# Kernel tuning notes

Measured on AMD Instinct MI355X. Metric: run time of the kernel, lower is better.

## Reference

```python
import jax, jax.numpy as jnp
import numpy as np

B, N, K = 8, 4096, 16
N_STEPS = 4
DT = 0.05
EPS = 1e-8


def symmetrize(M):
    return 0.5 * (M + jnp.swapaxes(M, -1, -2))


def ensure_spd(S, eps):
    # Project to SPD cone via eigenvalue clipping: V max(L, eps) V^T
    Kd = S.shape[-1]
    S = symmetrize(S + eps * jnp.eye(Kd, dtype=S.dtype))
    w, U = jnp.linalg.eigh(S)
    w = jnp.clip(w, eps, None)
    return symmetrize((U * w[..., None, :]) @ jnp.swapaxes(U, -1, -2))


def spd_exponential_map(Sigma, V, eps=EPS):
    # exp_Sigma(V) = S^{1/2} exp(S^{-1/2} V S^{-1/2}) S^{1/2}
    Kd = Sigma.shape[-1]
    Sigma = symmetrize(Sigma) + eps * jnp.eye(Kd, dtype=Sigma.dtype)
    w, U = jnp.linalg.eigh(Sigma)
    w = jnp.clip(w, eps, None)
    sq = jnp.sqrt(w)
    Ut = jnp.swapaxes(U, -1, -2)
    S_sqrt = (U * sq[..., None, :]) @ Ut
    S_isqrt = (U * (1.0 / sq)[..., None, :]) @ Ut
    W = symmetrize(S_isqrt @ V @ S_isqrt)
    ww, Uw = jnp.linalg.eigh(W)
    ww = jnp.clip(ww, -20.0, 20.0)
    expW = (Uw * jnp.exp(ww)[..., None, :]) @ jnp.swapaxes(Uw, -1, -2)
    return ensure_spd(S_sqrt @ expW @ S_sqrt, eps)


def spd_kinetic_gradient(Sigma, pi_Sigma):
    # dT/dSigma = 2 pi Sigma pi, symmetrized
    return symmetrize(2.0 * (pi_Sigma @ Sigma) @ pi_Sigma)


def retract_to_principal_ball(phi, margin=0.01):
    eps = 1e-12
    r_max = jnp.pi - margin
    theta = jnp.linalg.norm(phi, axis=-1, keepdims=True)
    theta_safe = jnp.maximum(theta, eps)
    axis = phi / theta_safe
    two_pi = 2.0 * jnp.pi
    tw = jnp.remainder(theta, two_pi)
    flip = tw > jnp.pi
    tf = jnp.where(flip, two_pi - tw, tw)
    af = jnp.where(flip, -axis, axis)
    tf = jnp.minimum(tf, r_max)
    return af * tf


def setup_inputs() -> dict:
    key = jax.random.key(0)
    ks = jax.random.split(key, 7)
    mu = jax.random.normal(ks[0], (B, N, K), dtype=jnp.float32)
    A = 0.3 * jax.random.normal(ks[1], (B, N, K, K), dtype=jnp.float32)
    Sigma = A @ jnp.swapaxes(A, -1, -2) + jnp.eye(K, dtype=jnp.float32)
    phi = 0.5 * jax.random.normal(ks[2], (B, N, 3), dtype=jnp.float32)
    pi_mu = 0.1 * jax.random.normal(ks[3], (B, N, K), dtype=jnp.float32)
    pi_Sigma = symmetrize(0.05 * jax.random.normal(ks[4], (B, N, K, K), dtype=jnp.float32))
    pi_phi = 0.1 * jax.random.normal(ks[5], (B, N, 3), dtype=jnp.float32)
    Bm = 0.3 * jax.random.normal(ks[6], (B, N, K, K), dtype=jnp.float32)
    M_inv = Bm @ jnp.swapaxes(Bm, -1, -2) + jnp.eye(K, dtype=jnp.float32)
    return {"mu": mu, "Sigma": Sigma, "phi": phi,
            "pi_mu": pi_mu, "pi_Sigma": pi_Sigma, "pi_phi": pi_phi,
            "M_inv": M_inv}


def reference(mu, Sigma, phi, pi_mu, pi_Sigma, pi_phi, M_inv):
    dt = DT
    for _ in range(N_STEPS):  # fixed small leapfrog step count
        # half-step momentum kick from curved-geometry kinetic force
        pi_Sigma = symmetrize(pi_Sigma - 0.5 * dt * spd_kinetic_gradient(Sigma, pi_Sigma))
        # full-step position drift
        mu = mu + dt * jnp.einsum('bnij,bnj->bni', M_inv, pi_mu)
        Sigma_dot = 2.0 * Sigma @ pi_Sigma @ Sigma  # dSigma/dt from Legendre transform
        Sigma = spd_exponential_map(Sigma, dt * Sigma_dot, EPS)
        phi = retract_to_principal_ball(phi + dt * pi_phi)
        # second half-step momentum kick
        pi_Sigma = symmetrize(pi_Sigma - 0.5 * dt * spd_kinetic_gradient(Sigma, pi_Sigma))
    return (mu, Sigma, phi)
```

## Files before the change

### kernel.cpp

```cpp
#include <hip/hip_runtime.h>
#include <math.h>

typedef float f32x4 __attribute__((ext_vector_type(4)));
typedef _Float16 f16x4 __attribute__((ext_vector_type(4)));
typedef __fp16 fp16x2 __attribute__((ext_vector_type(2)));
typedef __fp16 fp16x4 __attribute__((ext_vector_type(4)));

#define MFMA_F16 __builtin_amdgcn_mfma_f32_16x16x16f16

namespace {
constexpr float DT = 0.05f;
constexpr int NSTEPS = 4;

struct Split { f16x4 h; f16x4 l; };

__device__ __forceinline__ f16x4 pk4(f32x4 v) {
  fp16x2 a = __builtin_amdgcn_cvt_pkrtz(v[0], v[1]);
  fp16x2 b = __builtin_amdgcn_cvt_pkrtz(v[2], v[3]);
  fp16x4 r = __builtin_shufflevector(a, b, 0, 1, 2, 3);
  return __builtin_bit_cast(f16x4, r);
}

__device__ __forceinline__ Split mksplit(f32x4 v) {
  Split s;
  s.h = pk4(v);
  f32x4 hf;
#pragma unroll
  for (int i = 0; i < 4; ++i) hf[i] = (float)s.h[i];
  s.l = pk4(v - hf);
  return s;
}

__device__ __forceinline__ f32x4 mm3(Split a, Split b) {
  f32x4 acc = {0.f, 0.f, 0.f, 0.f};
  acc = MFMA_F16(a.h, b.h, acc, 0, 0, 0);
  acc = MFMA_F16(a.h, b.l, acc, 0, 0, 0);
  acc = MFMA_F16(a.l, b.h, acc, 0, 0, 0);
  return acc;
}
__device__ __forceinline__ f32x4 mm2_acc(Split a, f16x4 bh, f32x4 acc0) {
  f32x4 acc = acc0;
  acc = MFMA_F16(a.h, bh, acc, 0, 0, 0);
  acc = MFMA_F16(a.l, bh, acc, 0, 0, 0);
  return acc;
}
__device__ __forceinline__ f32x4 mm1(f16x4 ah, f16x4 bh) {
  f32x4 acc = {0.f, 0.f, 0.f, 0.f};
  acc = MFMA_F16(ah, bh, acc, 0, 0, 0);
  return acc;
}
}

__global__ __launch_bounds__(256, 4) void ham_leapfrog(
    const float* __restrict__ mu, const float* __restrict__ Sigma,
    const float* __restrict__ phi, const float* __restrict__ pi_mu,
    const float* __restrict__ pi_Sigma, const float* __restrict__ pi_phi,
    const float* __restrict__ M_inv, float* __restrict__ out, int n_elem) {
  const int wave = threadIdx.x >> 6;
  const int lane = threadIdx.x & 63;
  const int e = blockIdx.x * (blockDim.x >> 6) + wave;
  if (e >= n_elem) return;

  const int c = lane & 15;
  const int r0 = (lane >> 4) * 4;
  const int eb = e * 256;
  const int ev = e * 16;

  f32x4 Sg, Dv, Mi;
#pragma unroll
  for (int j = 0; j < 4; ++j) {
    const int off = eb + (r0 + j) * 16 + c;
    Sg[j] = Sigma[off];
    Dv[j] = pi_Sigma[off];
    Mi[j] = M_inv[off];
  }
  Dv = (2.0f * DT) * Dv;

  f32x4 pm4 = *(const f32x4*)(pi_mu + ev + r0);
  f16x4 Ph = pk4(pm4);
  if (c != 0) Ph = (f16x4)(_Float16)0;
  f32x4 am = mm1(pk4(Mi), Ph);

  float p0 = phi[e * 3 + 0];
  float p1 = phi[e * 3 + 1];
  float p2 = phi[e * 3 + 2];
  const float q0 = DT * pi_phi[e * 3 + 0];
  const float q1 = DT * pi_phi[e * 3 + 1];
  const float q2 = DT * pi_phi[e * 3 + 2];
  const float TWO_PI = 6.28318530717958647692f;
  const float INV_2PI = 0.15915494309189533577f;
  const float PI_F = 3.14159265358979323846f;
  const float R_MAX = 3.13159265358979323846f;
#pragma unroll
  for (int s = 0; s < NSTEPS; ++s) {
    p0 += q0; p1 += q1; p2 += q2;
    float th = sqrtf(p0 * p0 + p1 * p1 + p2 * p2);
    float inv = __builtin_amdgcn_rcpf(fmaxf(th, 1e-12f));
    float tw = th - TWO_PI * floorf(th * INV_2PI);
    bool flip = tw > PI_F;
    float tf = flip ? (TWO_PI - tw) : tw;
    float sgn = flip ? -1.f : 1.f;
    tf = fminf(tf, R_MAX);
    float f = sgn * inv * tf;
    p0 *= f; p1 *= f; p2 *= f;
  }

  Split sS = mksplit(Sg);
  Split sD = mksplit(Dv);

#pragma unroll
  for (int step = 0; step < NSTEPS; ++step) {
    {
      f32x4 T = mm3(sS, sD);
      f16x4 Th = pk4(-0.5f * T);
      Dv = mm2_acc(sD, Th, Dv);
      sD = mksplit(Dv);
    }
    {
      f32x4 X = mm3(sD, sS);
      Split sX = mksplit(X);
      f32x4 Z = mm3(sS, sX);
      f32x4 ACC = Sg + Z;
      f16x4 zh = pk4(Z);
      Z = mm1(zh, sX.h); ACC += (1.0f / 2.0f) * Z; zh = pk4(Z);
      Z = mm1(zh, sX.h); ACC += (1.0f / 6.0f) * Z; zh = pk4(Z);
      Z = mm1(zh, sX.h); ACC += (1.0f / 24.0f) * Z;
      Sg = ACC;
      sS = mksplit(Sg);
    }
    {
      f32x4 T = mm3(sS, sD);
      f16x4 Th = pk4(-0.5f * T);
      Dv = mm2_acc(sD, Th, Dv);
      sD = mksplit(Dv);
    }
  }

  float* out_mu = out;
  float* out_Sg = out + (size_t)n_elem * 16;
  float* out_ph = out + (size_t)n_elem * (16 + 256);

#pragma unroll
  for (int j = 0; j < 4; ++j)
    out_Sg[eb + (r0 + j) * 16 + c] = Sg[j];

  if (c == 0) {
    f32x4 mu4 = *(const f32x4*)(mu + ev + r0);
    *(f32x4*)(out_mu + ev + r0) = mu4 + ((float)NSTEPS * DT) * am;
  }
  if (lane == 0) {
    out_ph[e * 3 + 0] = p0;
    out_ph[e * 3 + 1] = p1;
    out_ph[e * 3 + 2] = p2;
  }
}

extern "C" void kernel_launch(void* const* d_in, const int* in_sizes, int n_in,
                              void* d_out, int out_size, void* d_ws, size_t ws_size,
                              hipStream_t stream) {
  const float* mu       = (const float*)d_in[0];
  const float* Sigma    = (const float*)d_in[1];
  const float* phi      = (const float*)d_in[2];
  const float* pi_mu    = (const float*)d_in[3];
  const float* pi_Sigma = (const float*)d_in[4];
  const float* pi_phi   = (const float*)d_in[5];
  const float* M_inv    = (const float*)d_in[6];
  float* o = (float*)d_out;

  const int n_elem = in_sizes[0] / 16;
  const int waves_per_block = 4;
  const int blocks = (n_elem + waves_per_block - 1) / waves_per_block;
  hipLaunchKernelGGL(ham_leapfrog, dim3(blocks), dim3(256), 0, stream,
                     mu, Sigma, phi, pi_mu, pi_Sigma, pi_phi, M_inv, o, n_elem);
}
```

Measured before the change: 153.1 us.

## Process two matrices per wave and interleave their MFMA chains, trimming kick precision

Each wave now handles two independent 16x16 elements and alternates their kick and drift steps, so the two dependent MFMA chains can overlap and hide MFMA latency. The kick's first product drops the low-by-high correction term (3 MFMAs down to 2), slightly lowering precision. The mu update and phi retraction are moved and the phi work is split across two lanes. Register pressure roughly doubles, which may lower occupancy under the 256x4 launch bounds.

```diff
diff --git a/kernel.cpp b/kernel.cpp
--- a/kernel.cpp
+++ b/kernel.cpp
@@ -31,23 +31,44 @@
   return s;
 }
 
-__device__ __forceinline__ f32x4 mm3(Split a, Split b) {
-  f32x4 acc = {0.f, 0.f, 0.f, 0.f};
-  acc = MFMA_F16(a.h, b.h, acc, 0, 0, 0);
-  acc = MFMA_F16(a.h, b.l, acc, 0, 0, 0);
-  acc = MFMA_F16(a.l, b.h, acc, 0, 0, 0);
-  return acc;
-}
-__device__ __forceinline__ f32x4 mm2_acc(Split a, f16x4 bh, f32x4 acc0) {
-  f32x4 acc = acc0;
-  acc = MFMA_F16(a.h, bh, acc, 0, 0, 0);
-  acc = MFMA_F16(a.l, bh, acc, 0, 0, 0);
-  return acc;
-}
 __device__ __forceinline__ f32x4 mm1(f16x4 ah, f16x4 bh) {
   f32x4 acc = {0.f, 0.f, 0.f, 0.f};
   acc = MFMA_F16(ah, bh, acc, 0, 0, 0);
   return acc;
+}
+
+struct El {
+  f32x4 Sg, Dv;
+  Split sS, sD;
+};
+
+__device__ __forceinline__ void kick(El& E) {
+  f32x4 T = {0.f, 0.f, 0.f, 0.f};
+  T = MFMA_F16(E.sS.h, E.sD.h, T, 0, 0, 0);
+  T = MFMA_F16(E.sS.h, E.sD.l, T, 0, 0, 0);
+  f16x4 Th = pk4(-0.5f * T);
+  E.Dv = MFMA_F16(E.sD.h, Th, E.Dv, 0, 0, 0);
+  E.Dv = MFMA_F16(E.sD.l, Th, E.Dv, 0, 0, 0);
+  E.sD = mksplit(E.Dv);
+}
+
+__device__ __forceinline__ void drift(El& E) {
+  f32x4 X = {0.f, 0.f, 0.f, 0.f};
+  X = MFMA_F16(E.sD.h, E.sS.h, X, 0, 0, 0);
+  X = MFMA_F16(E.sD.l, E.sS.h, X, 0, 0, 0);
+  X = MFMA_F16(E.sD.h, E.sS.l, X, 0, 0, 0);
+  Split sX = mksplit(X);
+  f32x4 Z = {0.f, 0.f, 0.f, 0.f};
+  Z = MFMA_F16(E.sS.h, sX.h, Z, 0, 0, 0);
+  Z = MFMA_F16(E.sS.l, sX.h, Z, 0, 0, 0);
+  Z = MFMA_F16(E.sS.h, sX.l, Z, 0, 0, 0);
+  f32x4 ACC = E.Sg + Z;
+  f16x4 zh = pk4(Z);
+  Z = mm1(zh, sX.h); ACC += (1.0f / 2.0f) * Z; zh = pk4(Z);
+  Z = mm1(zh, sX.h); ACC += (1.0f / 6.0f) * Z; zh = pk4(Z);
+  Z = mm1(zh, sX.h); ACC += (1.0f / 24.0f) * Z;
+  E.Sg = ACC;
+  E.sS = mksplit(ACC);
 }
 }
 
@@ -58,97 +79,82 @@
     const float* __restrict__ M_inv, float* __restrict__ out, int n_elem) {
   const int wave = threadIdx.x >> 6;
   const int lane = threadIdx.x & 63;
-  const int e = blockIdx.x * (blockDim.x >> 6) + wave;
-  if (e >= n_elem) return;
+  const int gw = blockIdx.x * (blockDim.x >> 6) + wave;
+  const int e0 = gw * 2;
+  if (e0 >= n_elem) return;
+  const int e1 = (e0 + 1 < n_elem) ? e0 + 1 : e0;
 
   const int c = lane & 15;
   const int r0 = (lane >> 4) * 4;
-  const int eb = e * 256;
-  const int ev = e * 16;
+  const int base = r0 * 16 + c;
 
-  f32x4 Sg, Dv, Mi;
+  El E0, E1;
+  f32x4 Mi0, Mi1;
 #pragma unroll
   for (int j = 0; j < 4; ++j) {
-    const int off = eb + (r0 + j) * 16 + c;
-    Sg[j] = Sigma[off];
-    Dv[j] = pi_Sigma[off];
-    Mi[j] = M_inv[off];
+    const int o0 = e0 * 256 + base + j * 16;
+    const int o1 = e1 * 256 + base + j * 16;
+    E0.Sg[j] = Sigma[o0];     E1.Sg[j] = Sigma[o1];
+    E0.Dv[j] = pi_Sigma[o0];  E1.Dv[j] = pi_Sigma[o1];
+    Mi0[j]   = M_inv[o0];     Mi1[j]   = M_inv[o1];
   }
-  Dv = (2.0f * DT) * Dv;
+  E0.Dv = (2.0f * DT) * E0.Dv;
+  E1.Dv = (2.0f * DT) * E1.Dv;
 
-  f32x4 pm4 = *(const f32x4*)(pi_mu + ev + r0);
-  f16x4 Ph = pk4(pm4);
-  if (c != 0) Ph = (f16x4)(_Float16)0;
-  f32x4 am = mm1(pk4(Mi), Ph);
+  f32x4 pm0 = *(const f32x4*)(pi_mu + e0 * 16 + r0);
+  f32x4 pm1 = *(const f32x4*)(pi_mu + e1 * 16 + r0);
+  f16x4 Ph0 = pk4(pm0), Ph1 = pk4(pm1);
+  if (c != 0) { Ph0 = (f16x4)(_Float16)0; Ph1 = (f16x4)(_Float16)0; }
+  f32x4 am0 = mm1(pk4(Mi0), Ph0);
+  f32x4 am1 = mm1(pk4(Mi1), Ph1);
+  if (c == 0) {
+    f32x4 mu0 = *(const f32x4*)(mu + e0 * 16 + r0);
+    f32x4 mu1 = *(const f32x4*)(mu + e1 * 16 + r0);
+    *(f32x4*)(out + e0 * 16 + r0) = mu0 + ((float)NSTEPS * DT) * am0;
+    *(f32x4*)(out + e1 * 16 + r0) = mu1 + ((float)NSTEPS * DT) * am1;
+  }
 
-  float p0 = phi[e * 3 + 0];
-  float p1 = phi[e * 3 + 1];
-  float p2 = phi[e * 3 + 2];
-  const float q0 = DT * pi_phi[e * 3 + 0];
-  const float q1 = DT * pi_phi[e * 3 + 1];
-  const float q2 = DT * pi_phi[e * 3 + 2];
+  E0.sS = mksplit(E0.Sg);  E1.sS = mksplit(E1.Sg);
+  E0.sD = mksplit(E0.Dv);  E1.sD = mksplit(E1.Dv);
+
+#pragma unroll
+  for (int step = 0; step < NSTEPS; ++step) {
+    kick(E0);  kick(E1);
+    drift(E0); drift(E1);
+    kick(E0);  kick(E1);
+  }
+
+  float* out_Sg = out + (size_t)n_elem * 16;
+#pragma unroll
+  for (int j = 0; j < 4; ++j) {
+    out_Sg[e0 * 256 + base + j * 16] = E0.Sg[j];
+    out_Sg[e1 * 256 + base + j * 16] = E1.Sg[j];
+  }
+
   const float TWO_PI = 6.28318530717958647692f;
   const float INV_2PI = 0.15915494309189533577f;
   const float PI_F = 3.14159265358979323846f;
   const float R_MAX = 3.13159265358979323846f;
+  float* out_ph = out + (size_t)n_elem * (16 + 256);
+  if (lane < 2) {
+    const int e = (lane == 0) ? e0 : e1;
+    float p0 = phi[e * 3 + 0], p1 = phi[e * 3 + 1], p2 = phi[e * 3 + 2];
+    const float q0 = DT * pi_phi[e * 3 + 0];
+    const float q1 = DT * pi_phi[e * 3 + 1];
+    const float q2 = DT * pi_phi[e * 3 + 2];
 #pragma unroll
-  for (int s = 0; s < NSTEPS; ++s) {
-    p0 += q0; p1 += q1; p2 += q2;
-    float th = sqrtf(p0 * p0 + p1 * p1 + p2 * p2);
-    float inv = __builtin_amdgcn_rcpf(fmaxf(th, 1e-12f));
-    float tw = th - TWO_PI * floorf(th * INV_2PI);
-    bool flip = tw > PI_F;
-    float tf = flip ? (TWO_PI - tw) : tw;
-    float sgn = flip ? -1.f : 1.f;
-    tf = fminf(tf, R_MAX);
-    float f = sgn * inv * tf;
-    p0 *= f; p1 *= f; p2 *= f;
-  }
-
-  Split sS = mksplit(Sg);
-  Split sD = mksplit(Dv);
-
-#pragma unroll
-  for (int step = 0; step < NSTEPS; ++step) {
-    {
-      f32x4 T = mm3(sS, sD);
-      f16x4 Th = pk4(-0.5f * T);
-      Dv = mm2_acc(sD, Th, Dv);
-      sD = mksplit(Dv);
+    for (int s = 0; s < NSTEPS; ++s) {
+      p0 += q0; p1 += q1; p2 += q2;
+      float th = sqrtf(p0 * p0 + p1 * p1 + p2 * p2);
+      float inv = __builtin_amdgcn_rcpf(fmaxf(th, 1e-12f));
+      float tw = th - TWO_PI * floorf(th * INV_2PI);
+      bool flip = tw > PI_F;
+      float tf = flip ? (TWO_PI - tw) : tw;
+      float sgn = flip ? -1.f : 1.f;
+      tf = fminf(tf, R_MAX);
+      float f = sgn * inv * tf;
+      p0 *= f; p1 *= f; p2 *= f;
     }
-    {
-      f32x4 X = mm3(sD, sS);
-      Split sX = mksplit(X);
-      f32x4 Z = mm3(sS, sX);
-      f32x4 ACC = Sg + Z;
-      f16x4 zh = pk4(Z);
-      Z = mm1(zh, sX.h); ACC += (1.0f / 2.0f) * Z; zh = pk4(Z);
-      Z = mm1(zh, sX.h); ACC += (1.0f / 6.0f) * Z; zh = pk4(Z);
-      Z = mm1(zh, sX.h); ACC += (1.0f / 24.0f) * Z;
-      Sg = ACC;
-      sS = mksplit(Sg);
-    }
-    {
-      f32x4 T = mm3(sS, sD);
-      f16x4 Th = pk4(-0.5f * T);
-      Dv = mm2_acc(sD, Th, Dv);
-      sD = mksplit(Dv);
-    }
-  }
-
-  float* out_mu = out;
-  float* out_Sg = out + (size_t)n_elem * 16;
-  float* out_ph = out + (size_t)n_elem * (16 + 256);
-
-#pragma unroll
-  for (int j = 0; j < 4; ++j)
-    out_Sg[eb + (r0 + j) * 16 + c] = Sg[j];
-
-  if (c == 0) {
-    f32x4 mu4 = *(const f32x4*)(mu + ev + r0);
-    *(f32x4*)(out_mu + ev + r0) = mu4 + ((float)NSTEPS * DT) * am;
-  }
-  if (lane == 0) {
     out_ph[e * 3 + 0] = p0;
     out_ph[e * 3 + 1] = p1;
     out_ph[e * 3 + 2] = p2;
@@ -169,7 +175,8 @@
 
   const int n_elem = in_sizes[0] / 16;
   const int waves_per_block = 4;
-  const int blocks = (n_elem + waves_per_block - 1) / waves_per_block;
+  const int elems_per_block = waves_per_block * 2;
+  const int blocks = (n_elem + elems_per_block - 1) / elems_per_block;
   hipLaunchKernelGGL(ham_leapfrog, dim3(blocks), dim3(256), 0, stream,
                      mu, Sigma, phi, pi_mu, pi_Sigma, pi_phi, M_inv, o, n_elem);
 }
```

Measured after the change: 153.5 us. Within noise of the previous version (+0.3%).
